# Kernel optimization log

Hardware: AMD Instinct MI355X
Metric: run time of the kernel (lower is better)

## Reference

```python
import jax, jax.numpy as jnp
import numpy as np
from jax import lax

B, T, IN_DIM, HID, K_WIN, N_TAGS, N_LAYERS = 128, 1024, 42, 256, 11, 8, 5
PAD = K_WIN // 2


def conv1d(x, w, b, pad):
    # x: (B, C_in, T), w: (C_out, C_in, K) -> (B, C_out, T)
    out = lax.conv_general_dilated(x, w, (1,), [(pad, pad)],
                                   dimension_numbers=('NCH', 'OIH', 'NCH'))
    return out + b[None, :, None]


def setup_inputs() -> dict:
    key = jax.random.key(0)
    ks = jax.random.split(key, 20)
    inp = {}
    inp['x'] = jax.random.normal(ks[0], (B, T, IN_DIM), dtype=jnp.float32)
    inp['lengths'] = jnp.full((B,), T, dtype=jnp.int32)
    inp['mask'] = jnp.ones((B, T), dtype=bool)
    inp['tags'] = jax.random.randint(ks[1], (B, T), 0, N_TAGS).astype(jnp.int32)
    prev = IN_DIM
    for i in range(N_LAYERS):
        scale = 1.0 / np.sqrt(prev * K_WIN)
        inp[f'w{i}'] = jax.random.uniform(ks[2 + i], (HID, prev, K_WIN), minval=-scale, maxval=scale, dtype=jnp.float32)
        inp[f'b{i}'] = jax.random.uniform(ks[8 + i], (HID,), minval=-scale, maxval=scale, dtype=jnp.float32)
        prev = HID
    scale = 1.0 / np.sqrt(HID)
    inp['w_out'] = jax.random.uniform(ks[14], (N_TAGS, HID, 1), minval=-scale, maxval=scale, dtype=jnp.float32)
    inp['b_out'] = jax.random.uniform(ks[15], (N_TAGS,), minval=-scale, maxval=scale, dtype=jnp.float32)
    # torchcrf initializes transitions uniform(-0.1, 0.1)
    inp['start_trans'] = jax.random.uniform(ks[16], (N_TAGS,), minval=-0.1, maxval=0.1, dtype=jnp.float32)
    inp['end_trans'] = jax.random.uniform(ks[17], (N_TAGS,), minval=-0.1, maxval=0.1, dtype=jnp.float32)
    inp['trans'] = jax.random.uniform(ks[18], (N_TAGS, N_TAGS), minval=-0.1, maxval=0.1, dtype=jnp.float32)
    return inp


def _emissions(x, ws, bs, w_out, b_out):
    h = jnp.transpose(x, (0, 2, 1))  # (B, C, T)
    for w, b in zip(ws, bs):
        h = jnp.tanh(conv1d(h, w, b, PAD))
    em = conv1d(h, w_out, b_out, 0)  # (B, K, T)
    return jnp.transpose(em, (0, 2, 1))  # (B, T, K)


def _crf_nll(emissions, tags, mask, start_trans, end_trans, trans):
    # loss = -sum_b log p(tags_b | emissions_b); torchcrf reduction='sum'
    Bn = emissions.shape[0]
    maskf = mask.astype(emissions.dtype)
    idx_b = jnp.arange(Bn)
    # --- numerator: path score of gold tags ---
    score0 = start_trans[tags[:, 0]] + emissions[idx_b, 0, tags[:, 0]]
    em_rest = jnp.transpose(emissions[:, 1:], (1, 0, 2))   # (T-1, B, K)
    tag_rest = tags[:, 1:].T                                # (T-1, B)
    m_rest = maskf[:, 1:].T                                 # (T-1, B)

    def num_step(carry, inp):
        score, prev_tag = carry
        em_t, tag_t, m_t = inp
        step = trans[prev_tag, tag_t] + em_t[idx_b, tag_t]
        score = score + step * m_t
        prev_tag = jnp.where(m_t > 0, tag_t, prev_tag)
        return (score, prev_tag), None

    (score, last_tag), _ = lax.scan(num_step, (score0, tags[:, 0]), (em_rest, tag_rest, m_rest))
    score = score + end_trans[last_tag]
    # --- denominator: forward algorithm (log partition) ---
    alpha0 = start_trans[None, :] + emissions[:, 0]  # (B, K)

    def den_step(alpha, inp):
        em_t, m_t = inp
        nxt = jax.nn.logsumexp(alpha[:, :, None] + trans[None, :, :] + em_t[:, None, :], axis=1)
        return jnp.where(m_t[:, None] > 0, nxt, alpha), None

    alpha, _ = lax.scan(den_step, alpha0, (em_rest, m_rest))
    log_z = jax.nn.logsumexp(alpha + end_trans[None, :], axis=1)
    return -jnp.sum(score - log_z)


def reference(x, lengths, mask, tags, w0, b0, w1, b1, w2, b2, w3, b3, w4, b4,
              w_out, b_out, start_trans, end_trans, trans):
    em = _emissions(x, [w0, w1, w2, w3, w4], [b0, b1, b2, b3, b4], w_out, b_out)
    return _crf_nll(em, tags, mask, start_trans, end_trans, trans)
```

## Files before the change

### kernel.cpp

```cpp
#include <hip/hip_runtime.h>


#define B_ 128
#define T_ 1024
#define IN_DIM_ 42
#define HID_ 256
#define KW_ 11
#define NTAGS_ 8
#define SEG_ 32
#define SEGL_ (T_ / SEG_)

typedef __bf16 bf16x8 __attribute__((ext_vector_type(8)));
typedef float f32x4 __attribute__((ext_vector_type(4)));
typedef short s16x8 __attribute__((ext_vector_type(8)));
typedef int i32x4 __attribute__((ext_vector_type(4)));
typedef int i32x8 __attribute__((ext_vector_type(8)));

struct i4pair { i32x4 lo, hi; };
__device__ __forceinline__ i32x8 mk8(i32x4 lo, i32x4 hi) {
    i4pair p{lo, hi};
    return __builtin_bit_cast(i32x8, p);
}

__device__ __forceinline__ unsigned short f2bf(float f) {
    unsigned u = __builtin_bit_cast(unsigned, f);
    u += 0x7FFFu + ((u >> 16) & 1u);
    return (unsigned short)(u >> 16);
}
__device__ __forceinline__ float fast_tanh(float x) {
    float e = __expf(2.f * x);
    return 1.f - 2.f / (e + 1.f);
}
__device__ __forceinline__ unsigned char f2fp8(float v) {
    return (unsigned char)(__builtin_amdgcn_cvt_pk_fp8_f32(v, v, 0, false) & 0xff);
}

#define SZ0_ (KW_ * 2 * 16 * 512)
#define SZF8_ (22 * 16 * 64 * 32)

__global__ void pack_l0(const float* __restrict__ w0, unsigned short* __restrict__ wp) {
    for (int idx = blockIdx.x * 256 + threadIdx.x; idx < SZ0_;
         idx += gridDim.x * 256) {
        int it2 = idx >> 13;
        int cic = it2 & 1, k = it2 >> 1;
        int e    = idx & 7;
        int lane = (idx >> 3) & 63;
        int coc  = (idx >> 9) & 15;
        int co = coc * 16 + (lane & 15);
        int ci = cic * 32 + ((lane >> 4) & 3) * 8 + e;
        float v = (ci < IN_DIM_) ? w0[(co * IN_DIM_ + ci) * KW_ + k] : 0.f;
        wp[idx] = f2bf(v);
    }
}

__global__ void pack_f8(const float* __restrict__ w1, const float* __restrict__ w2,
                        const float* __restrict__ w3, const float* __restrict__ w4,
                        unsigned char* __restrict__ wp8) {
    const int total = 4 * SZF8_;
    for (int idx = blockIdx.x * 256 + threadIdx.x; idx < total;
         idx += gridDim.x * 256) {
        int L   = idx / SZF8_;
        int loc = idx - L * SZF8_;
        const float* w = (L == 0) ? w1 : (L == 1) ? w2 : (L == 2) ? w3 : w4;
        int e    = loc & 31;
        int lane = (loc >> 5) & 63;
        int coc  = (loc >> 11) & 15;
        int it   = loc >> 15;
        int cic  = it / KW_;
        int k    = it - cic * KW_;
        int co = coc * 16 + (lane & 15);
        int ci = cic * 128 + (lane >> 4) * 32 + e;
        wp8[idx] = f2fp8(256.f * w[(co * HID_ + ci) * KW_ + k]);
    }
}

__global__ __launch_bounds__(512, 4)
void conv_first(const float* __restrict__ x, const unsigned short* __restrict__ wpack,
                const float* __restrict__ bias, unsigned char* __restrict__ out) {
    constexpr int CIN = 64, ROWS = 138;
    __shared__ unsigned short lds[ROWS * CIN];

    const int tid  = threadIdx.x;
    const int wave = tid >> 6;
    const int lane = tid & 63;
    const int l15  = lane & 15;
    const int lhi  = lane >> 4;
    const int wr   = wave >> 2;
    const int wc   = wave & 3;
    const int b    = blockIdx.x >> 3;
    const int t0   = (blockIdx.x & 7) * 128;

    for (int u = tid; u < ROWS * 32; u += 512) {
        int r = u >> 5, m = u & 31;
        int gt = t0 - 5 + r;
        unsigned val = 0;
        if (gt >= 0 && gt < T_ && 2 * m < IN_DIM_) {
            float2 f = *(const float2*)&x[((size_t)b * T_ + gt) * IN_DIM_ + 2 * m];
            val = (unsigned)f2bf(f.x) | ((unsigned)f2bf(f.y) << 16);
        }
        int c = m >> 2;
        int p = c ^ ((r + 3) & 7);
        ((unsigned*)lds)[(r * CIN + p * 8) / 2 + (m & 3)] = val;
    }
    __syncthreads();

    f32x4 acc[4][4];
#pragma unroll
    for (int tf = 0; tf < 4; ++tf)
#pragma unroll
        for (int n = 0; n < 4; ++n) acc[tf][n] = (f32x4){0.f, 0.f, 0.f, 0.f};

    const unsigned short* wpq = wpack + (size_t)(wc * 4) * 512 + lane * 8;
    const int arow = (wr * 64 + l15) * CIN;
    const int l153 = l15 + 3;

    s16x8 Bq[2][4];
#pragma unroll
    for (int n = 0; n < 4; ++n) Bq[0][n] = *(const s16x8*)&wpq[n * 512];

#pragma unroll
    for (int k = 0; k < KW_; ++k) {
#pragma unroll
        for (int cic = 0; cic < 2; ++cic) {
            const int it2 = k * 2 + cic;
            const int nxt = it2 + 1;
#pragma unroll
            for (int n = 0; n < 4; ++n)
                Bq[nxt & 1][n] = *(const s16x8*)&wpq[(size_t)nxt * 8192 + n * 512];
            const int key = (l153 + k) & 7;
            const int ao  = arow + (((cic * 4 + lhi) ^ key) << 3);
            s16x8 a0 = *(const s16x8*)&lds[ao + (0 * 16 + k) * CIN];
            s16x8 a1 = *(const s16x8*)&lds[ao + (1 * 16 + k) * CIN];
            s16x8 a2 = *(const s16x8*)&lds[ao + (2 * 16 + k) * CIN];
            s16x8 a3 = *(const s16x8*)&lds[ao + (3 * 16 + k) * CIN];
            __builtin_amdgcn_s_setprio(1);
#pragma unroll
            for (int n = 0; n < 4; ++n) {
                bf16x8 bb = __builtin_bit_cast(bf16x8, Bq[it2 & 1][n]);
                acc[0][n] = __builtin_amdgcn_mfma_f32_16x16x32_bf16(
                    __builtin_bit_cast(bf16x8, a0), bb, acc[0][n], 0, 0, 0);
                acc[1][n] = __builtin_amdgcn_mfma_f32_16x16x32_bf16(
                    __builtin_bit_cast(bf16x8, a1), bb, acc[1][n], 0, 0, 0);
                acc[2][n] = __builtin_amdgcn_mfma_f32_16x16x32_bf16(
                    __builtin_bit_cast(bf16x8, a2), bb, acc[2][n], 0, 0, 0);
                acc[3][n] = __builtin_amdgcn_mfma_f32_16x16x32_bf16(
                    __builtin_bit_cast(bf16x8, a3), bb, acc[3][n], 0, 0, 0);
            }
            __builtin_amdgcn_s_setprio(0);
        }
    }

#pragma unroll
    for (int n = 0; n < 4; ++n) {
        int co = wc * 64 + n * 16 + l15;
        float bv = bias[co];
        int cch = co >> 4, cby = co & 15;
#pragma unroll
        for (int tf = 0; tf < 4; ++tf) {
#pragma unroll
            for (int r4 = 0; r4 < 4; ++r4) {
                int t = t0 + wr * 64 + tf * 16 + lhi * 4 + r4;
                float v = fast_tanh(acc[tf][n][r4] + bv);
                out[((size_t)b * T_ + t) * 256 + ((cch ^ (t & 15)) << 4) + cby] =
                    f2fp8(v);
            }
        }
    }
}

template <bool LAST>
__global__ __launch_bounds__(256, 2)
void conv_mid(const unsigned char* __restrict__ Hin,
              const unsigned char* __restrict__ wpack,
              const float* __restrict__ bias, unsigned char* __restrict__ out,
              const float* __restrict__ w_out, float* __restrict__ emout) {
    extern __shared__ unsigned char lds8[];

    const int tid  = threadIdx.x;
    const int wave = tid >> 6;
    const int lane = tid & 63;
    const int l15  = lane & 15;
    const int lhi  = lane >> 4;
    const int wc   = wave;
    const int b    = blockIdx.x >> 3;
    const int t0   = (blockIdx.x & 7) * 128;

    for (int c = wave; c < 35; c += 4) {
        int r0 = c * 4;
        int r  = r0 + (lane >> 4);
        int gt = t0 - 5 + r;
        gt = gt < 0 ? 0 : (gt >= T_ ? T_ - 1 : gt);
        const unsigned char* src =
            Hin + ((size_t)b * T_ + gt) * 256 + (lane & 15) * 16;
        __builtin_amdgcn_global_load_lds(
            (const __attribute__((address_space(1))) void*)src,
            (__attribute__((address_space(3))) void*)&lds8[r0 * 256], 16, 0, 0);
    }
    __syncthreads();
    if (t0 == 0) {
        for (int u = tid; u < 320; u += 256)
            ((unsigned*)lds8)[u] = 0;
    }
    if (t0 == T_ - 128) {
        for (int u = tid; u < 320; u += 256)
            ((unsigned*)&lds8[133 * 256])[u] = 0;
    }
    __syncthreads();

    f32x4 acc[8][4];
#pragma unroll
    for (int tf = 0; tf < 8; ++tf)
#pragma unroll
        for (int n = 0; n < 4; ++n) acc[tf][n] = (f32x4){0.f, 0.f, 0.f, 0.f};

    const unsigned char* wpB = wpack + (size_t)(wc * 4) * 2048 + lane * 32;

    i32x8 Aa[8], Bs0, Bs1;

#define LOAD_BS(SLOT, itv, nv)                                                 \
    {                                                                          \
        const unsigned char* p_ = wpB + (size_t)(itv) * 32768 + (nv) * 2048;   \
        SLOT = mk8(*(const i32x4*)p_, *(const i32x4*)(p_ + 16));               \
    }
#define CL(BS, n_)                                                             \
    {                                                                          \
        __builtin_amdgcn_s_setprio(1);                                         \
        _Pragma("unroll") for (int tf = 0; tf < 8; ++tf)                       \
            acc[tf][n_] = __builtin_amdgcn_mfma_scale_f32_16x16x128_f8f6f4(    \
                Aa[tf], BS, acc[tf][n_], 0, 0,                                 \
                0, 0x7F7F7F7F, 0, 0x7F7F7F7F);               \
        __builtin_amdgcn_s_setprio(0);                                         \
    }

    LOAD_BS(Bs0, 0, 0);
    LOAD_BS(Bs1, 0, 1);

#pragma unroll 1
    for (int kk = 0; kk < 22; ++kk) {
        const int cic_ = kk / KW_;
        const int kn_  = kk - cic_ * KW_;
        const int key_ = (l15 + kn_ + 11) & 15;
        const int ca_  = ((cic_ * 8 + lhi * 2) ^ key_) << 4;
        const int rb_  = (l15 + kn_) * 256 + ca_;
#pragma unroll
        for (int tf = 0; tf < 8; ++tf)
            Aa[tf] = mk8(*(const i32x4*)&lds8[rb_ + tf * 4096],
                         *(const i32x4*)&lds8[(rb_ + tf * 4096) ^ 16]);
        CL(Bs0, 0); LOAD_BS(Bs0, kk, 2);
        CL(Bs1, 1); LOAD_BS(Bs1, kk, 3);
        CL(Bs0, 2); LOAD_BS(Bs0, kk + 1, 0);
        CL(Bs1, 3); LOAD_BS(Bs1, kk + 1, 1);
    }
#undef LOAD_BS
#undef CL

    constexpr float INV = 1.f / 256.f;
    if constexpr (!LAST) {
#pragma unroll
        for (int n = 0; n < 4; ++n) {
            int co = wc * 64 + n * 16 + l15;
            float bv = bias[co];
            int cch = co >> 4, cby = co & 15;
#pragma unroll
            for (int tf = 0; tf < 8; ++tf) {
#pragma unroll
                for (int r4 = 0; r4 < 4; ++r4) {
                    int t = t0 + tf * 16 + lhi * 4 + r4;
                    float v = fast_tanh(acc[tf][n][r4] * INV + bv);
                    out[((size_t)b * T_ + t) * 256 + ((cch ^ (t & 15)) << 4) + cby] =
                        f2fp8(v);
                }
            }
        }
    } else {
        float wv[4][NTAGS_], bvn[4];
#pragma unroll
        for (int n = 0; n < 4; ++n) {
            int co = wc * 64 + n * 16 + l15;
            bvn[n] = bias[co];
#pragma unroll
            for (int tg = 0; tg < NTAGS_; ++tg) wv[n][tg] = w_out[tg * HID_ + co];
        }
        __syncthreads();
        float* pbuf = (float*)lds8;
#pragma unroll
        for (int tf = 0; tf < 8; ++tf) {
#pragma unroll
            for (int r4 = 0; r4 < 4; ++r4) {
                float h[4];
#pragma unroll
                for (int n = 0; n < 4; ++n)
                    h[n] = fast_tanh(acc[tf][n][r4] * INV + bvn[n]);
                float pt[NTAGS_];
#pragma unroll
                for (int tg = 0; tg < NTAGS_; ++tg)
                    pt[tg] = h[0] * wv[0][tg] + h[1] * wv[1][tg] +
                             h[2] * wv[2][tg] + h[3] * wv[3][tg];
#pragma unroll
                for (int off = 8; off; off >>= 1)
#pragma unroll
                    for (int tg = 0; tg < NTAGS_; ++tg)
                        pt[tg] += __shfl_down(pt[tg], off);
                if (l15 == 0) {
                    int tloc = tf * 16 + lhi * 4 + r4;
                    f32x4 lo = {pt[0], pt[1], pt[2], pt[3]};
                    f32x4 hi = {pt[4], pt[5], pt[6], pt[7]};
                    *(f32x4*)&pbuf[(wc * 128 + tloc) * 8]     = lo;
                    *(f32x4*)&pbuf[(wc * 128 + tloc) * 8 + 4] = hi;
                }
            }
        }
        __syncthreads();
        for (int u = tid; u < 128 * NTAGS_; u += 256) {
            float s = pbuf[u] + pbuf[1024 + u] + pbuf[2048 + u] + pbuf[3072 + u];
            emout[((size_t)b * T_ + t0) * NTAGS_ + u] = s;
        }
    }
}

__global__ __launch_bounds__(256)
void crf_seg_kernel(const float* __restrict__ em, const float* __restrict__ tr,
                    const float* __restrict__ bo, float* __restrict__ segM) {
    const int gw   = blockIdx.x * 4 + (threadIdx.x >> 6);
    const int b    = gw >> 5;
    const int s    = gw & 31;
    const int lane = threadIdx.x & 63;
    const int i    = lane >> 3;
    const int j    = lane & 7;
    const float* emb = em + (size_t)b * T_ * NTAGS_;
    const float boj = bo[j];

    float tc[8];
#pragma unroll
    for (int k = 0; k < 8; ++k) tc[k] = tr[k * 8 + j];

    const int tb = (s == 0) ? 1 : s * SEGL_;
    const int te = (s + 1) * SEGL_;

    float m = tr[i * 8 + j] + emb[tb * 8 + j] + boj;
    for (int t = tb + 1; t < te; ++t) {
        float emt = emb[t * 8 + j] + boj;
        float v[8];
#pragma unroll
        for (int k = 0; k < 8; ++k) v[k] = __shfl(m, (lane & 56) + k) + tc[k];
        float mx = fmaxf(fmaxf(fmaxf(v[0], v[1]), fmaxf(v[2], v[3])),
                         fmaxf(fmaxf(v[4], v[5]), fmaxf(v[6], v[7])));
        float sm = 0.f;
#pragma unroll
        for (int k = 0; k < 8; ++k) sm += __expf(v[k] - mx);
        m = mx + __logf(sm) + emt;
    }
    segM[(size_t)gw * 64 + lane] = m;
}

__global__ __launch_bounds__(64)
void crf_kernel(const float* __restrict__ em, const float* __restrict__ segM,
                const int* __restrict__ tags,
                const float* __restrict__ st, const float* __restrict__ et,
                const float* __restrict__ tr, const float* __restrict__ bo,
                float* __restrict__ outp) {
    __shared__ float sM[SEG_ * 64];
    const int b    = blockIdx.x;
    const int lane = threadIdx.x;
    const float* emb = em + (size_t)b * T_ * NTAGS_;
    const int*   tg  = tags + (size_t)b * T_;

    for (int u = lane; u < SEG_ * 64; u += 64)
        sM[u] = segM[(size_t)b * SEG_ * 64 + u];

    const float breg = bo[lane & 7];

    float num = 0.f;
    for (int t = 1 + lane; t < T_; t += 64) {
        int pt = tg[t - 1], ct = tg[t];
        num += tr[pt * NTAGS_ + ct] + emb[t * NTAGS_ + ct] + __shfl(breg, ct);
    }
#pragma unroll
    for (int off = 32; off; off >>= 1) num += __shfl_down(num, off);
    int tgf = tg[0], tgl = tg[T_ - 1];
    float bo_f = __shfl(breg, tgf);
    float score = 0.f;
    if (lane == 0)
        score = num + st[tgf] + emb[tgf] + bo_f + et[tgl];

    __syncthreads();

    const int j = lane & 7;
    float alpha = st[j] + emb[j] + breg;
    for (int sgm = 0; sgm < SEG_; ++sgm) {
        const float* M = &sM[sgm * 64];
        float v[8];
#pragma unroll
        for (int i = 0; i < 8; ++i) v[i] = __shfl(alpha, i) + M[i * 8 + j];
        float mx = fmaxf(fmaxf(fmaxf(v[0], v[1]), fmaxf(v[2], v[3])),
                         fmaxf(fmaxf(v[4], v[5]), fmaxf(v[6], v[7])));
        float sm = 0.f;
#pragma unroll
        for (int i = 0; i < 8; ++i) sm += __expf(v[i] - mx);
        alpha = mx + __logf(sm);
    }
    float vj = alpha + et[j];
    float w[8];
#pragma unroll
    for (int i = 0; i < 8; ++i) w[i] = __shfl(vj, i);
    float m2 = w[0];
#pragma unroll
    for (int i = 1; i < 8; ++i) m2 = fmaxf(m2, w[i]);
    float s2 = 0.f;
#pragma unroll
    for (int i = 0; i < 8; ++i) s2 += __expf(w[i] - m2);
    float log_z = m2 + __logf(s2);

    if (lane == 0) atomicAdd(outp, log_z - score);
}

extern "C" void kernel_launch(void* const* d_in, const int* in_sizes, int n_in,
                              void* d_out, int out_size, void* d_ws, size_t ws_size,
                              hipStream_t stream) {
    const float* x     = (const float*)d_in[0];
    const int*   tags  = (const int*)d_in[3];
    const float* w[5]  = {(const float*)d_in[4], (const float*)d_in[6],
                          (const float*)d_in[8], (const float*)d_in[10],
                          (const float*)d_in[12]};
    const float* bias[5] = {(const float*)d_in[5], (const float*)d_in[7],
                            (const float*)d_in[9], (const float*)d_in[11],
                            (const float*)d_in[13]};
    const float* w_out = (const float*)d_in[14];
    const float* b_out = (const float*)d_in[15];
    const float* st    = (const float*)d_in[16];
    const float* et    = (const float*)d_in[17];
    const float* tr    = (const float*)d_in[18];

    unsigned char* H0 = (unsigned char*)d_ws;
    unsigned char* H1 = H0 + (size_t)B_ * T_ * 256;
    unsigned short* wp0 = (unsigned short*)(H1 + (size_t)B_ * T_ * 256);
    unsigned char* wpf8 = (unsigned char*)(wp0 + SZ0_);
    float* em   = (float*)(wpf8 + 4 * (size_t)SZF8_);
    float* segM = em + (size_t)B_ * T_ * NTAGS_;

    pack_l0<<<176, 256, 0, stream>>>(w[0], wp0);
    pack_f8<<<2048, 256, 0, stream>>>(w[1], w[2], w[3], w[4], wpf8);

    conv_first<<<B_ * (T_ / 128), 512, 0, stream>>>(x, wp0, bias[0], H0);

    const int NBLK = B_ * (T_ / 128);
    const int MLDS = 140 * 256;
    unsigned char* wpl[4] = {wpf8, wpf8 + SZF8_, wpf8 + 2 * (size_t)SZF8_,
                             wpf8 + 3 * (size_t)SZF8_};
    conv_mid<false><<<NBLK, 256, MLDS, stream>>>(H0, wpl[0], bias[1], H1,
                                                 nullptr, nullptr);
    conv_mid<false><<<NBLK, 256, MLDS, stream>>>(H1, wpl[1], bias[2], H0,
                                                 nullptr, nullptr);
    conv_mid<false><<<NBLK, 256, MLDS, stream>>>(H0, wpl[2], bias[3], H1,
                                                 nullptr, nullptr);
    conv_mid<true><<<NBLK, 256, MLDS, stream>>>(H1, wpl[3], bias[4], nullptr,
                                                w_out, em);

    crf_seg_kernel<<<B_ * SEG_ / 4, 256, 0, stream>>>(em, tr, b_out, segM);

    hipMemsetAsync(d_out, 0, sizeof(float), stream);
    crf_kernel<<<B_, 64, 0, stream>>>(em, segM, tags, st, et, tr, b_out,
                                      (float*)d_out);
}
```

Measured before the change: 454.0 us.

## Double-buffer LDS A-fragment reads in halves to overlap with MFMA

```diff
diff --git a/kernel.cpp b/kernel.cpp
--- a/kernel.cpp
+++ b/kernel.cpp
@@ -215,44 +215,65 @@
 
     const unsigned char* wpB = wpack + (size_t)(wc * 4) * 2048 + lane * 32;
 
-    i32x8 Aa[8], Bs0, Bs1;
-
-#define LOAD_BS(SLOT, itv, nv)                                                 \
+    i32x8 Aa[4], Ab[4], Bq[4];
+
+#define RB_OF(itv)                                                             \
+    ({                                                                         \
+        const int it_  = (itv) > 21 ? 21 : (itv);                              \
+        const int cic_ = it_ / KW_;                                            \
+        const int kn_  = it_ - cic_ * KW_;                                     \
+        const int key_ = (l15 + kn_ + 11) & 15;                                \
+        (l15 + kn_) * 256 + (((cic_ * 8 + lhi * 2) ^ key_) << 4);              \
+    })
+#define READ_A4(BUF, rbv, TB)                                                  \
+    {                                                                          \
+        _Pragma("unroll") for (int j = 0; j < 4; ++j) {                        \
+            const int ad_ = (rbv) + (TB + j) * 4096;                           \
+            BUF[j] = mk8(*(const i32x4*)&lds8[ad_],                            \
+                         *(const i32x4*)&lds8[ad_ ^ 16]);                      \
+        }                                                                      \
+    }
+#define CL4(BUF, n_, TB)                                                       \
+    {                                                                          \
+        __builtin_amdgcn_s_setprio(1);                                         \
+        _Pragma("unroll") for (int j = 0; j < 4; ++j)                          \
+            acc[TB + j][n_] = __builtin_amdgcn_mfma_scale_f32_16x16x128_f8f6f4(\
+                BUF[j], Bq[n_], acc[TB + j][n_], 0, 0,                         \
+                0, 0x7F7F7F7F, 0, 0x7F7F7F7F);               \
+        __builtin_amdgcn_s_setprio(0);                                         \
+    }
+#define LOAD_B(nv, itv)                                                        \
     {                                                                          \
         const unsigned char* p_ = wpB + (size_t)(itv) * 32768 + (nv) * 2048;   \
-        SLOT = mk8(*(const i32x4*)p_, *(const i32x4*)(p_ + 16));               \
-    }
-#define CL(BS, n_)                                                             \
-    {                                                                          \
-        __builtin_amdgcn_s_setprio(1);                                         \
-        _Pragma("unroll") for (int tf = 0; tf < 8; ++tf)                       \
-            acc[tf][n_] = __builtin_amdgcn_mfma_scale_f32_16x16x128_f8f6f4(    \
-                Aa[tf], BS, acc[tf][n_], 0, 0,                                 \
-                0, 0x7F7F7F7F, 0, 0x7F7F7F7F);               \
-        __builtin_amdgcn_s_setprio(0);                                         \
-    }
-
-    LOAD_BS(Bs0, 0, 0);
-    LOAD_BS(Bs1, 0, 1);
+        Bq[nv] = mk8(*(const i32x4*)p_, *(const i32x4*)(p_ + 16));             \
+    }
+
+    {
+        const int rb0 = RB_OF(0);
+        READ_A4(Aa, rb0, 0);
+    }
+#pragma unroll
+    for (int n = 0; n < 4; ++n) LOAD_B(n, 0);
 
 #pragma unroll 1
     for (int kk = 0; kk < 22; ++kk) {
-        const int cic_ = kk / KW_;
-        const int kn_  = kk - cic_ * KW_;
-        const int key_ = (l15 + kn_ + 11) & 15;
-        const int ca_  = ((cic_ * 8 + lhi * 2) ^ key_) << 4;
-        const int rb_  = (l15 + kn_) * 256 + ca_;
-#pragma unroll
-        for (int tf = 0; tf < 8; ++tf)
-            Aa[tf] = mk8(*(const i32x4*)&lds8[rb_ + tf * 4096],
-                         *(const i32x4*)&lds8[(rb_ + tf * 4096) ^ 16]);
-        CL(Bs0, 0); LOAD_BS(Bs0, kk, 2);
-        CL(Bs1, 1); LOAD_BS(Bs1, kk, 3);
-        CL(Bs0, 2); LOAD_BS(Bs0, kk + 1, 0);
-        CL(Bs1, 3); LOAD_BS(Bs1, kk + 1, 1);
-    }
-#undef LOAD_BS
-#undef CL
+        const int rb_ = RB_OF(kk);
+        READ_A4(Ab, rb_, 4);
+        CL4(Aa, 0, 0);
+        CL4(Aa, 1, 0);
+        CL4(Aa, 2, 0);
+        CL4(Aa, 3, 0);
+        const int rbn_ = RB_OF(kk + 1);
+        READ_A4(Aa, rbn_, 0);
+        CL4(Ab, 0, 4); LOAD_B(0, kk + 1);
+        CL4(Ab, 1, 4); LOAD_B(1, kk + 1);
+        CL4(Ab, 2, 4); LOAD_B(2, kk + 1);
+        CL4(Ab, 3, 4); LOAD_B(3, kk + 1);
+    }
+#undef RB_OF
+#undef READ_A4
+#undef CL4
+#undef LOAD_B
 
     constexpr float INV = 1.f / 256.f;
     if constexpr (!LAST) {
```

Measured after the change: 457.3 us. No clear change (+0.7%).

## Switch first conv layer from bf16 MFMA to fp8 scaled MFMA with tap pairing

Applied to the files above, without the earlier changes.

```diff
diff --git a/kernel.cpp b/kernel.cpp
--- a/kernel.cpp
+++ b/kernel.cpp
@@ -10,9 +10,7 @@
 #define SEG_ 32
 #define SEGL_ (T_ / SEG_)
 
-typedef __bf16 bf16x8 __attribute__((ext_vector_type(8)));
 typedef float f32x4 __attribute__((ext_vector_type(4)));
-typedef short s16x8 __attribute__((ext_vector_type(8)));
 typedef int i32x4 __attribute__((ext_vector_type(4)));
 typedef int i32x8 __attribute__((ext_vector_type(8)));
 
@@ -22,11 +20,6 @@
     return __builtin_bit_cast(i32x8, p);
 }
 
-__device__ __forceinline__ unsigned short f2bf(float f) {
-    unsigned u = __builtin_bit_cast(unsigned, f);
-    u += 0x7FFFu + ((u >> 16) & 1u);
-    return (unsigned short)(u >> 16);
-}
 __device__ __forceinline__ float fast_tanh(float x) {
     float e = __expf(2.f * x);
     return 1.f - 2.f / (e + 1.f);
@@ -35,21 +28,23 @@
     return (unsigned char)(__builtin_amdgcn_cvt_pk_fp8_f32(v, v, 0, false) & 0xff);
 }
 
-#define SZ0_ (KW_ * 2 * 16 * 512)
-#define SZF8_ (22 * 16 * 64 * 32)
-
-__global__ void pack_l0(const float* __restrict__ w0, unsigned short* __restrict__ wp) {
-    for (int idx = blockIdx.x * 256 + threadIdx.x; idx < SZ0_;
+#define SZ0F8_ (6 * 16 * 64 * 32)
+#define SZF8_  (22 * 16 * 64 * 32)
+
+__global__ void pack_l0f8(const float* __restrict__ w0, unsigned char* __restrict__ wp) {
+    for (int idx = blockIdx.x * 256 + threadIdx.x; idx < SZ0F8_;
          idx += gridDim.x * 256) {
-        int it2 = idx >> 13;
-        int cic = it2 & 1, k = it2 >> 1;
-        int e    = idx & 7;
-        int lane = (idx >> 3) & 63;
-        int coc  = (idx >> 9) & 15;
-        int co = coc * 16 + (lane & 15);
-        int ci = cic * 32 + ((lane >> 4) & 3) * 8 + e;
-        float v = (ci < IN_DIM_) ? w0[(co * IN_DIM_ + ci) * KW_ + k] : 0.f;
-        wp[idx] = f2bf(v);
+        int e    = idx & 31;
+        int lane = (idx >> 5) & 63;
+        int coc  = (idx >> 11) & 15;
+        int it   = idx >> 15;
+        int kq   = (lane >> 4) * 32 + e;
+        int tap  = 2 * it + (kq >> 6);
+        int c    = kq & 63;
+        int co   = coc * 16 + (lane & 15);
+        float v = (tap < KW_ && c < IN_DIM_)
+                      ? 256.f * w0[(co * IN_DIM_ + c) * KW_ + tap] : 0.f;
+        wp[idx] = f2fp8(v);
     }
 }
 
@@ -75,10 +70,9 @@
 }
 
 __global__ __launch_bounds__(512, 4)
-void conv_first(const float* __restrict__ x, const unsigned short* __restrict__ wpack,
+void conv_first(const float* __restrict__ x, const unsigned char* __restrict__ wpack,
                 const float* __restrict__ bias, unsigned char* __restrict__ out) {
-    constexpr int CIN = 64, ROWS = 138;
-    __shared__ unsigned short lds[ROWS * CIN];
+    __shared__ unsigned char lds8[139 * 80];
 
     const int tid  = threadIdx.x;
     const int wave = tid >> 6;
@@ -90,17 +84,19 @@
     const int b    = blockIdx.x >> 3;
     const int t0   = (blockIdx.x & 7) * 128;
 
-    for (int u = tid; u < ROWS * 32; u += 512) {
-        int r = u >> 5, m = u & 31;
+    for (int u = tid; u < 139 * 16; u += 512) {
+        int r = u >> 4, q = u & 15;
         int gt = t0 - 5 + r;
-        unsigned val = 0;
-        if (gt >= 0 && gt < T_ && 2 * m < IN_DIM_) {
-            float2 f = *(const float2*)&x[((size_t)b * T_ + gt) * IN_DIM_ + 2 * m];
-            val = (unsigned)f2bf(f.x) | ((unsigned)f2bf(f.y) << 16);
-        }
-        int c = m >> 2;
-        int p = c ^ ((r + 3) & 7);
-        ((unsigned*)lds)[(r * CIN + p * 8) / 2 + (m & 3)] = val;
+        unsigned pk = 0;
+        if (gt >= 0 && gt < T_) {
+            const float* xr = &x[((size_t)b * T_ + gt) * IN_DIM_];
+#pragma unroll
+            for (int j = 0; j < 4; ++j) {
+                int c = q * 4 + j;
+                if (c < IN_DIM_) pk |= (unsigned)f2fp8(xr[c]) << (8 * j);
+            }
+        }
+        *(unsigned*)&lds8[r * 80 + q * 4] = pk;
     }
     __syncthreads();
 
@@ -110,46 +106,45 @@
 #pragma unroll
         for (int n = 0; n < 4; ++n) acc[tf][n] = (f32x4){0.f, 0.f, 0.f, 0.f};
 
-    const unsigned short* wpq = wpack + (size_t)(wc * 4) * 512 + lane * 8;
-    const int arow = (wr * 64 + l15) * CIN;
-    const int l153 = l15 + 3;
-
-    s16x8 Bq[2][4];
-#pragma unroll
-    for (int n = 0; n < 4; ++n) Bq[0][n] = *(const s16x8*)&wpq[n * 512];
-
-#pragma unroll
-    for (int k = 0; k < KW_; ++k) {
-#pragma unroll
-        for (int cic = 0; cic < 2; ++cic) {
-            const int it2 = k * 2 + cic;
-            const int nxt = it2 + 1;
-#pragma unroll
-            for (int n = 0; n < 4; ++n)
-                Bq[nxt & 1][n] = *(const s16x8*)&wpq[(size_t)nxt * 8192 + n * 512];
-            const int key = (l153 + k) & 7;
-            const int ao  = arow + (((cic * 4 + lhi) ^ key) << 3);
-            s16x8 a0 = *(const s16x8*)&lds[ao + (0 * 16 + k) * CIN];
-            s16x8 a1 = *(const s16x8*)&lds[ao + (1 * 16 + k) * CIN];
-            s16x8 a2 = *(const s16x8*)&lds[ao + (2 * 16 + k) * CIN];
-            s16x8 a3 = *(const s16x8*)&lds[ao + (3 * 16 + k) * CIN];
-            __builtin_amdgcn_s_setprio(1);
-#pragma unroll
-            for (int n = 0; n < 4; ++n) {
-                bf16x8 bb = __builtin_bit_cast(bf16x8, Bq[it2 & 1][n]);
-                acc[0][n] = __builtin_amdgcn_mfma_f32_16x16x32_bf16(
-                    __builtin_bit_cast(bf16x8, a0), bb, acc[0][n], 0, 0, 0);
-                acc[1][n] = __builtin_amdgcn_mfma_f32_16x16x32_bf16(
-                    __builtin_bit_cast(bf16x8, a1), bb, acc[1][n], 0, 0, 0);
-                acc[2][n] = __builtin_amdgcn_mfma_f32_16x16x32_bf16(
-                    __builtin_bit_cast(bf16x8, a2), bb, acc[2][n], 0, 0, 0);
-                acc[3][n] = __builtin_amdgcn_mfma_f32_16x16x32_bf16(
-                    __builtin_bit_cast(bf16x8, a3), bb, acc[3][n], 0, 0, 0);
-            }
-            __builtin_amdgcn_s_setprio(0);
-        }
-    }
-
+    const unsigned char* wpB = wpack + (size_t)(wc * 4) * 2048 + lane * 32;
+    const int abase0 = (wr * 64 + l15 + (lhi >> 1)) * 80 + (lhi & 1) * 32;
+
+    i32x8 Aa[4], Bs0, Bs1;
+
+#define LOAD_BS(SLOT, itv, nv)                                                 \
+    {                                                                          \
+        const unsigned char* p_ = wpB + (size_t)(itv) * 32768 + (nv) * 2048;   \
+        SLOT = mk8(*(const i32x4*)p_, *(const i32x4*)(p_ + 16));               \
+    }
+#define CL(BS, n_)                                                             \
+    {                                                                          \
+        __builtin_amdgcn_s_setprio(1);                                         \
+        _Pragma("unroll") for (int tf = 0; tf < 4; ++tf)                       \
+            acc[tf][n_] = __builtin_amdgcn_mfma_scale_f32_16x16x128_f8f6f4(    \
+                Aa[tf], BS, acc[tf][n_], 0, 0,                                 \
+                0, 0x7F7F7F7F, 0, 0x7F7F7F7F);               \
+        __builtin_amdgcn_s_setprio(0);                                         \
+    }
+
+    LOAD_BS(Bs0, 0, 0);
+    LOAD_BS(Bs1, 0, 1);
+
+#pragma unroll
+    for (int it = 0; it < 6; ++it) {
+        const int ab = abase0 + it * 160;
+#pragma unroll
+        for (int tf = 0; tf < 4; ++tf)
+            Aa[tf] = mk8(*(const i32x4*)&lds8[ab + tf * 1280],
+                         *(const i32x4*)&lds8[ab + tf * 1280 + 16]);
+        CL(Bs0, 0); LOAD_BS(Bs0, it, 2);
+        CL(Bs1, 1); LOAD_BS(Bs1, it, 3);
+        CL(Bs0, 2); LOAD_BS(Bs0, it + 1, 0);
+        CL(Bs1, 3); LOAD_BS(Bs1, it + 1, 1);
+    }
+#undef LOAD_BS
+#undef CL
+
+    constexpr float INV = 1.f / 256.f;
 #pragma unroll
     for (int n = 0; n < 4; ++n) {
         int co = wc * 64 + n * 16 + l15;
@@ -160,7 +155,7 @@
 #pragma unroll
             for (int r4 = 0; r4 < 4; ++r4) {
                 int t = t0 + wr * 64 + tf * 16 + lhi * 4 + r4;
-                float v = fast_tanh(acc[tf][n][r4] + bv);
+                float v = fast_tanh(acc[tf][n][r4] * INV + bv);
                 out[((size_t)b * T_ + t) * 256 + ((cch ^ (t & 15)) << 4) + cby] =
                     f2fp8(v);
             }
@@ -433,12 +428,12 @@
 
     unsigned char* H0 = (unsigned char*)d_ws;
     unsigned char* H1 = H0 + (size_t)B_ * T_ * 256;
-    unsigned short* wp0 = (unsigned short*)(H1 + (size_t)B_ * T_ * 256);
-    unsigned char* wpf8 = (unsigned char*)(wp0 + SZ0_);
+    unsigned char* wp0 = H1 + (size_t)B_ * T_ * 256;
+    unsigned char* wpf8 = wp0 + SZ0F8_;
     float* em   = (float*)(wpf8 + 4 * (size_t)SZF8_);
     float* segM = em + (size_t)B_ * T_ * NTAGS_;
 
-    pack_l0<<<176, 256, 0, stream>>>(w[0], wp0);
+    pack_l0f8<<<768, 256, 0, stream>>>(w[0], wp0);
     pack_f8<<<2048, 256, 0, stream>>>(w[1], w[2], w[3], w[4], wpf8);
 
     conv_first<<<B_ * (T_ / 128), 512, 0, stream>>>(x, wp0, bias[0], H0);
```

After: 459.2 us. No clear change (+1.1%).

## Split middle conv waves along time instead of output channels

Applied to the files above, without the earlier changes.

```diff
diff --git a/kernel.cpp b/kernel.cpp
--- a/kernel.cpp
+++ b/kernel.cpp
@@ -168,12 +168,10 @@
     }
 }
 
-template <bool LAST>
 __global__ __launch_bounds__(256, 2)
-void conv_mid(const unsigned char* __restrict__ Hin,
-              const unsigned char* __restrict__ wpack,
-              const float* __restrict__ bias, unsigned char* __restrict__ out,
-              const float* __restrict__ w_out, float* __restrict__ emout) {
+void conv_mid_t(const unsigned char* __restrict__ Hin,
+                const unsigned char* __restrict__ wpack,
+                const float* __restrict__ bias, unsigned char* __restrict__ out) {
     extern __shared__ unsigned char lds8[];
 
     const int tid  = threadIdx.x;
@@ -181,7 +179,6 @@
     const int lane = tid & 63;
     const int l15  = lane & 15;
     const int lhi  = lane >> 4;
-    const int wc   = wave;
     const int b    = blockIdx.x >> 3;
     const int t0   = (blockIdx.x & 7) * 128;
 
@@ -207,6 +204,120 @@
     }
     __syncthreads();
 
+    f32x4 acc[2][16];
+#pragma unroll
+    for (int tf = 0; tf < 2; ++tf)
+#pragma unroll
+        for (int n = 0; n < 16; ++n) acc[tf][n] = (f32x4){0.f, 0.f, 0.f, 0.f};
+
+    const unsigned char* wpB = wpack + lane * 32;
+    const int wbase = wave * 32;
+
+    i32x8 Aa0, Aa1, Bs0, Bs1;
+
+#define LOAD_BS(SLOT, itv, nv)                                                 \
+    {                                                                          \
+        const unsigned char* p_ = wpB + (size_t)(itv) * 32768 + (nv) * 2048;   \
+        SLOT = mk8(*(const i32x4*)p_, *(const i32x4*)(p_ + 16));               \
+    }
+#define CL(BS, n_)                                                             \
+    {                                                                          \
+        __builtin_amdgcn_s_setprio(1);                                         \
+        acc[0][n_] = __builtin_amdgcn_mfma_scale_f32_16x16x128_f8f6f4(         \
+            Aa0, BS, acc[0][n_], 0, 0, 0, 0x7F7F7F7F, 0, 0x7F7F7F7F);          \
+        acc[1][n_] = __builtin_amdgcn_mfma_scale_f32_16x16x128_f8f6f4(         \
+            Aa1, BS, acc[1][n_], 0, 0, 0, 0x7F7F7F7F, 0, 0x7F7F7F7F);          \
+        __builtin_amdgcn_s_setprio(0);                                         \
+    }
+
+    LOAD_BS(Bs0, 0, 0);
+    LOAD_BS(Bs1, 0, 1);
+
+#pragma unroll 1
+    for (int kk = 0; kk < 22; ++kk) {
+        const int cic_ = kk / KW_;
+        const int kn_  = kk - cic_ * KW_;
+        const int key_ = (l15 + kn_ + 11) & 15;
+        const int ca_  = ((cic_ * 8 + lhi * 2) ^ key_) << 4;
+        const int rb_  = (wbase + l15 + kn_) * 256 + ca_;
+        Aa0 = mk8(*(const i32x4*)&lds8[rb_], *(const i32x4*)&lds8[rb_ ^ 16]);
+        Aa1 = mk8(*(const i32x4*)&lds8[rb_ + 4096],
+                  *(const i32x4*)&lds8[(rb_ + 4096) ^ 16]);
+        CL(Bs0, 0);  LOAD_BS(Bs0, kk, 2);
+        CL(Bs1, 1);  LOAD_BS(Bs1, kk, 3);
+        CL(Bs0, 2);  LOAD_BS(Bs0, kk, 4);
+        CL(Bs1, 3);  LOAD_BS(Bs1, kk, 5);
+        CL(Bs0, 4);  LOAD_BS(Bs0, kk, 6);
+        CL(Bs1, 5);  LOAD_BS(Bs1, kk, 7);
+        CL(Bs0, 6);  LOAD_BS(Bs0, kk, 8);
+        CL(Bs1, 7);  LOAD_BS(Bs1, kk, 9);
+        CL(Bs0, 8);  LOAD_BS(Bs0, kk, 10);
+        CL(Bs1, 9);  LOAD_BS(Bs1, kk, 11);
+        CL(Bs0, 10); LOAD_BS(Bs0, kk, 12);
+        CL(Bs1, 11); LOAD_BS(Bs1, kk, 13);
+        CL(Bs0, 12); LOAD_BS(Bs0, kk, 14);
+        CL(Bs1, 13); LOAD_BS(Bs1, kk, 15);
+        CL(Bs0, 14); LOAD_BS(Bs0, kk + 1, 0);
+        CL(Bs1, 15); LOAD_BS(Bs1, kk + 1, 1);
+    }
+#undef LOAD_BS
+#undef CL
+
+    constexpr float INV = 1.f / 256.f;
+#pragma unroll
+    for (int n = 0; n < 16; ++n) {
+        float bv = bias[n * 16 + l15];
+#pragma unroll
+        for (int tf = 0; tf < 2; ++tf) {
+#pragma unroll
+            for (int r4 = 0; r4 < 4; ++r4) {
+                int t = t0 + wbase + tf * 16 + lhi * 4 + r4;
+                float v = fast_tanh(acc[tf][n][r4] * INV + bv);
+                out[((size_t)b * T_ + t) * 256 + ((n ^ (t & 15)) << 4) + l15] =
+                    f2fp8(v);
+            }
+        }
+    }
+}
+
+__global__ __launch_bounds__(256, 2)
+void conv_last(const unsigned char* __restrict__ Hin,
+               const unsigned char* __restrict__ wpack,
+               const float* __restrict__ bias,
+               const float* __restrict__ w_out, float* __restrict__ emout) {
+    extern __shared__ unsigned char lds8[];
+
+    const int tid  = threadIdx.x;
+    const int wave = tid >> 6;
+    const int lane = tid & 63;
+    const int l15  = lane & 15;
+    const int lhi  = lane >> 4;
+    const int wc   = wave;
+    const int b    = blockIdx.x >> 3;
+    const int t0   = (blockIdx.x & 7) * 128;
+
+    for (int c = wave; c < 35; c += 4) {
+        int r0 = c * 4;
+        int r  = r0 + (lane >> 4);
+        int gt = t0 - 5 + r;
+        gt = gt < 0 ? 0 : (gt >= T_ ? T_ - 1 : gt);
+        const unsigned char* src =
+            Hin + ((size_t)b * T_ + gt) * 256 + (lane & 15) * 16;
+        __builtin_amdgcn_global_load_lds(
+            (const __attribute__((address_space(1))) void*)src,
+            (__attribute__((address_space(3))) void*)&lds8[r0 * 256], 16, 0, 0);
+    }
+    __syncthreads();
+    if (t0 == 0) {
+        for (int u = tid; u < 320; u += 256)
+            ((unsigned*)lds8)[u] = 0;
+    }
+    if (t0 == T_ - 128) {
+        for (int u = tid; u < 320; u += 256)
+            ((unsigned*)&lds8[133 * 256])[u] = 0;
+    }
+    __syncthreads();
+
     f32x4 acc[8][4];
 #pragma unroll
     for (int tf = 0; tf < 8; ++tf)
@@ -228,7 +339,7 @@
         _Pragma("unroll") for (int tf = 0; tf < 8; ++tf)                       \
             acc[tf][n_] = __builtin_amdgcn_mfma_scale_f32_16x16x128_f8f6f4(    \
                 Aa[tf], BS, acc[tf][n_], 0, 0,                                 \
-                0, 0x7F7F7F7F, 0, 0x7F7F7F7F);               \
+                0, 0x7F7F7F7F, 0, 0x7F7F7F7F);                                 \
         __builtin_amdgcn_s_setprio(0);                                         \
     }
 
@@ -255,66 +366,47 @@
 #undef CL
 
     constexpr float INV = 1.f / 256.f;
-    if constexpr (!LAST) {
-#pragma unroll
-        for (int n = 0; n < 4; ++n) {
-            int co = wc * 64 + n * 16 + l15;
-            float bv = bias[co];
-            int cch = co >> 4, cby = co & 15;
-#pragma unroll
-            for (int tf = 0; tf < 8; ++tf) {
-#pragma unroll
-                for (int r4 = 0; r4 < 4; ++r4) {
-                    int t = t0 + tf * 16 + lhi * 4 + r4;
-                    float v = fast_tanh(acc[tf][n][r4] * INV + bv);
-                    out[((size_t)b * T_ + t) * 256 + ((cch ^ (t & 15)) << 4) + cby] =
-                        f2fp8(v);
-                }
+    float wv[4][NTAGS_], bvn[4];
+#pragma unroll
+    for (int n = 0; n < 4; ++n) {
+        int co = wc * 64 + n * 16 + l15;
+        bvn[n] = bias[co];
+#pragma unroll
+        for (int tg = 0; tg < NTAGS_; ++tg) wv[n][tg] = w_out[tg * HID_ + co];
+    }
+    __syncthreads();
+    float* pbuf = (float*)lds8;
+#pragma unroll
+    for (int tf = 0; tf < 8; ++tf) {
+#pragma unroll
+        for (int r4 = 0; r4 < 4; ++r4) {
+            float h[4];
+#pragma unroll
+            for (int n = 0; n < 4; ++n)
+                h[n] = fast_tanh(acc[tf][n][r4] * INV + bvn[n]);
+            float pt[NTAGS_];
+#pragma unroll
+            for (int tg = 0; tg < NTAGS_; ++tg)
+                pt[tg] = h[0] * wv[0][tg] + h[1] * wv[1][tg] +
+                         h[2] * wv[2][tg] + h[3] * wv[3][tg];
+#pragma unroll
+            for (int off = 8; off; off >>= 1)
+#pragma unroll
+                for (int tg = 0; tg < NTAGS_; ++tg)
+                    pt[tg] += __shfl_down(pt[tg], off);
+            if (l15 == 0) {
+                int tloc = tf * 16 + lhi * 4 + r4;
+                f32x4 lo = {pt[0], pt[1], pt[2], pt[3]};
+                f32x4 hi = {pt[4], pt[5], pt[6], pt[7]};
+                *(f32x4*)&pbuf[(wc * 128 + tloc) * 8]     = lo;
+                *(f32x4*)&pbuf[(wc * 128 + tloc) * 8 + 4] = hi;
             }
         }
-    } else {
-        float wv[4][NTAGS_], bvn[4];
-#pragma unroll
-        for (int n = 0; n < 4; ++n) {
-            int co = wc * 64 + n * 16 + l15;
-            bvn[n] = bias[co];
-#pragma unroll
-            for (int tg = 0; tg < NTAGS_; ++tg) wv[n][tg] = w_out[tg * HID_ + co];
-        }
-        __syncthreads();
-        float* pbuf = (float*)lds8;
-#pragma unroll
-        for (int tf = 0; tf < 8; ++tf) {
-#pragma unroll
-            for (int r4 = 0; r4 < 4; ++r4) {
-                float h[4];
-#pragma unroll
-                for (int n = 0; n < 4; ++n)
-                    h[n] = fast_tanh(acc[tf][n][r4] * INV + bvn[n]);
-                float pt[NTAGS_];
-#pragma unroll
-                for (int tg = 0; tg < NTAGS_; ++tg)
-                    pt[tg] = h[0] * wv[0][tg] + h[1] * wv[1][tg] +
-                             h[2] * wv[2][tg] + h[3] * wv[3][tg];
-#pragma unroll
-                for (int off = 8; off; off >>= 1)
-#pragma unroll
-                    for (int tg = 0; tg < NTAGS_; ++tg)
-                        pt[tg] += __shfl_down(pt[tg], off);
-                if (l15 == 0) {
-                    int tloc = tf * 16 + lhi * 4 + r4;
-                    f32x4 lo = {pt[0], pt[1], pt[2], pt[3]};
-                    f32x4 hi = {pt[4], pt[5], pt[6], pt[7]};
-                    *(f32x4*)&pbuf[(wc * 128 + tloc) * 8]     = lo;
-                    *(f32x4*)&pbuf[(wc * 128 + tloc) * 8 + 4] = hi;
-                }
-            }
-        }
-        __syncthreads();
-        for (int u = tid; u < 128 * NTAGS_; u += 256) {
-            float s = pbuf[u] + pbuf[1024 + u] + pbuf[2048 + u] + pbuf[3072 + u];
-            emout[((size_t)b * T_ + t0) * NTAGS_ + u] = s;
-        }
+    }
+    __syncthreads();
+    for (int u = tid; u < 128 * NTAGS_; u += 256) {
+        float s = pbuf[u] + pbuf[1024 + u] + pbuf[2048 + u] + pbuf[3072 + u];
+        emout[((size_t)b * T_ + t0) * NTAGS_ + u] = s;
     }
 }
 
@@ -447,14 +539,10 @@
     const int MLDS = 140 * 256;
     unsigned char* wpl[4] = {wpf8, wpf8 + SZF8_, wpf8 + 2 * (size_t)SZF8_,
                              wpf8 + 3 * (size_t)SZF8_};
-    conv_mid<false><<<NBLK, 256, MLDS, stream>>>(H0, wpl[0], bias[1], H1,
-                                                 nullptr, nullptr);
-    conv_mid<false><<<NBLK, 256, MLDS, stream>>>(H1, wpl[1], bias[2], H0,
-                                                 nullptr, nullptr);
-    conv_mid<false><<<NBLK, 256, MLDS, stream>>>(H0, wpl[2], bias[3], H1,
-                                                 nullptr, nullptr);
-    conv_mid<true><<<NBLK, 256, MLDS, stream>>>(H1, wpl[3], bias[4], nullptr,
-                                                w_out, em);
+    conv_mid_t<<<NBLK, 256, MLDS, stream>>>(H0, wpl[0], bias[1], H1);
+    conv_mid_t<<<NBLK, 256, MLDS, stream>>>(H1, wpl[1], bias[2], H0);
+    conv_mid_t<<<NBLK, 256, MLDS, stream>>>(H0, wpl[2], bias[3], H1);
+    conv_last<<<NBLK, 256, MLDS, stream>>>(H1, wpl[3], bias[4], w_out, em);
 
     crf_seg_kernel<<<B_ * SEG_ / 4, 256, 0, stream>>>(em, tr, b_out, segM);
 
```

Measured after the change: 573.6 us. 1.26x slower.
